# Performance work log

Measured on AMD Instinct MI355X. Metric: run time of the kernel, lower is better.

## Reference

```python
import jax, jax.numpy as jnp
import numpy as np

B, N_IN, D_IN = 64, 2304, 8
J, L = 32, 16  # num_capsules, capsule_dim
ROUTING_ITERS = 3
EPS = 1e-7


def setup_inputs() -> dict:
    key = jax.random.key(0)
    k1, k2 = jax.random.split(key)
    x = jax.random.normal(k1, (B, N_IN, D_IN), dtype=jnp.float32)
    W = jax.random.normal(k2, (N_IN, J, D_IN, L), dtype=jnp.float32) * 0.05
    return {"x": x, "W": W}


def squash(s):
    # s: [B, J, L]
    sq_norm = jnp.sum(jnp.square(s), axis=-1, keepdims=True)
    scale = sq_norm / (1.0 + sq_norm) / jnp.sqrt(sq_norm + EPS)
    return scale * s


def reference(x, W):
    # Faithful to the source: einsum 'bni,njkl->bnjl' sums i and k independently.
    predictions = jnp.einsum('bni,njkl->bnjl', x, W)  # [B, N, J, L]
    b = jnp.zeros((x.shape[0], N_IN, J), dtype=predictions.dtype)
    v = None
    for i in range(ROUTING_ITERS):
        c = jax.nn.softmax(b, axis=2)                       # [B, N, J]
        s = jnp.sum(predictions * c[..., None], axis=1)     # [B, J, L]
        v = squash(s)                                       # [B, J, L]
        if i < ROUTING_ITERS - 1:
            agreement = jnp.einsum('bnjl,bjl->bnj', predictions, v)
            b = b + agreement
    return v
```

## Files before the change

### kernel.cpp

```cpp
#include <hip/hip_runtime.h>

#define B_   64
#define N_   2304
#define J_   32
#define L_   16
#define EPS_ 1e-7f
#define BG   4
#define NSPL 16
#define NSL  144
#define NTHR 1024
#define NT   18
#define STR  20

__global__ __launch_bounds__(256) void prep_kernel(const float* __restrict__ x,
                                                   const float* __restrict__ W,
                                                   float* __restrict__ Ws,
                                                   float* __restrict__ xs_g) {
    const int o = blockIdx.x * 256 + threadIdx.x;
    const int NW4 = N_ * J_ * L_ / 4;
    if (o < NW4) {
        const int n = o >> 7, r = o & 127;
        const float4* base = (const float4*)W + (size_t)n * 1024 + (r >> 2) * 32 + (r & 3);
        float4 s = make_float4(0.f, 0.f, 0.f, 0.f);
#pragma unroll
        for (int k = 0; k < 8; ++k) {
            float4 t = base[k * 4];
            s.x += t.x; s.y += t.y; s.z += t.z; s.w += t.w;
        }
        ((float4*)Ws)[o] = s;
    } else {
        const int q = o - NW4;
        if (q < B_ * N_) {
            const float4* p4 = (const float4*)(x + (size_t)q * 8);
            float4 a = p4[0], c = p4[1];
            xs_g[q] = a.x + a.y + a.z + a.w + c.x + c.y + c.z + c.w;
        }
    }
}

template<int T>
__global__ __launch_bounds__(NTHR) void iter_kernel(const float* __restrict__ Ws,
                                                    const float* __restrict__ xs_g,
                                                    const float* __restrict__ pA,
                                                    const float* __restrict__ pB,
                                                    float* __restrict__ pout) {
    __shared__ float xs_lds[BG * NSL];
    __shared__ float u_lds[BG * 544];
    __shared__ float sred[512 * STR];

    const int tid = threadIdx.x;
    const int sp  = blockIdx.x & 15;
    const int bg  = blockIdx.x >> 4;
    const int bb  = bg * BG;
    const int nb  = sp * NSL;

    if (tid < BG * NSL) {
        const int b4f = tid / NSL, nlf = tid - b4f * NSL;
        xs_lds[tid] = xs_g[(size_t)(bb + b4f) * N_ + nb + nlf];
    }

    if constexpr (T > 0) {
        for (int q = tid; q < BG * 512; q += NTHR) {
            const int ob = q >> 9, jl = q & 511;
            const float* pp = pA + ((size_t)(bb + ob) * NSPL) * 512 + jl;
            float s = 0.f;
#pragma unroll
            for (int s2 = 0; s2 < NSPL; ++s2) s += pp[s2 * 512];
            float sq = s * s;
#pragma unroll
            for (int off = 1; off <= 8; off <<= 1) sq += __shfl_xor(sq, off);
            float u = s * (sq / (1.f + sq) / sqrtf(sq + EPS_));
            if constexpr (T == 2) {
                const float* pq = pB + ((size_t)(bb + ob) * NSPL) * 512 + jl;
                float s1 = 0.f;
#pragma unroll
                for (int s2 = 0; s2 < NSPL; ++s2) s1 += pq[s2 * 512];
                float sq1 = s1 * s1;
#pragma unroll
                for (int off = 1; off <= 8; off <<= 1) sq1 += __shfl_xor(sq1, off);
                u += s1 * (sq1 / (1.f + sq1) / sqrtf(sq1 + EPS_));
            }
            u_lds[ob * 544 + (jl >> 4) * 17 + (jl & 15)] = u;
        }
    }
    __syncthreads();

    const int nl8 = tid >> 7;
    const int b4  = (tid >> 5) & 3;
    const int j   = tid & 31;

    float u4[16];
    if constexpr (T > 0) {
#pragma unroll
        for (int l = 0; l < 16; ++l) u4[l] = u_lds[b4 * 544 + j * 17 + l];
    }

    float acc[16];
#pragma unroll
    for (int l = 0; l < 16; ++l) acc[l] = 0.f;

    const float* wbase = Ws + (size_t)nb * 512 + j * 16;
    const float* xbase = xs_lds + b4 * NSL;

    for (int tile = 0; tile < NT; ++tile) {
        const int nl = tile * 8 + nl8;
        const float4* wr = (const float4*)(wbase + (size_t)nl * 512);
        float4 w0 = wr[0], w1 = wr[1], w2 = wr[2], w3 = wr[3];
        const float xsv = xbase[nl];
        float wgt;
        if constexpr (T == 0) {
            wgt = xsv * (1.f / 32.f);
        } else {
            float lg = w0.x*u4[0]  + w0.y*u4[1]  + w0.z*u4[2]  + w0.w*u4[3]
                     + w1.x*u4[4]  + w1.y*u4[5]  + w1.z*u4[6]  + w1.w*u4[7]
                     + w2.x*u4[8]  + w2.y*u4[9]  + w2.z*u4[10] + w2.w*u4[11]
                     + w3.x*u4[12] + w3.y*u4[13] + w3.z*u4[14] + w3.w*u4[15];
            lg *= xsv;
            float e = __expf(lg);
            float ss = e;
#pragma unroll
            for (int off = 1; off <= 16; off <<= 1) ss += __shfl_xor(ss, off);
            wgt = (e / ss) * xsv;
        }
        acc[0]  += wgt*w0.x; acc[1]  += wgt*w0.y; acc[2]  += wgt*w0.z; acc[3]  += wgt*w0.w;
        acc[4]  += wgt*w1.x; acc[5]  += wgt*w1.y; acc[6]  += wgt*w1.z; acc[7]  += wgt*w1.w;
        acc[8]  += wgt*w2.x; acc[9]  += wgt*w2.y; acc[10] += wgt*w2.z; acc[11] += wgt*w2.w;
        acc[12] += wgt*w3.x; acc[13] += wgt*w3.y; acc[14] += wgt*w3.z; acc[15] += wgt*w3.w;
    }

    if (nl8 >= 4) {
        float* sr = sred + (size_t)(tid - 512) * STR;
        ((float4*)sr)[0] = make_float4(acc[0],  acc[1],  acc[2],  acc[3]);
        ((float4*)sr)[1] = make_float4(acc[4],  acc[5],  acc[6],  acc[7]);
        ((float4*)sr)[2] = make_float4(acc[8],  acc[9],  acc[10], acc[11]);
        ((float4*)sr)[3] = make_float4(acc[12], acc[13], acc[14], acc[15]);
    }
    __syncthreads();
    if (nl8 < 4) {
        float* sr = sred + (size_t)tid * STR;
#pragma unroll
        for (int d = 0; d < 4; ++d) {
            float4 t = ((float4*)sr)[d];
            t.x += acc[d*4+0]; t.y += acc[d*4+1]; t.z += acc[d*4+2]; t.w += acc[d*4+3];
            ((float4*)sr)[d] = t;
        }
    }
    __syncthreads();

    for (int q = tid; q < BG * 512; q += NTHR) {
        const int ob = q >> 9, jl = q & 511;
        const int oj = jl >> 4, ol = jl & 15;
        float s = 0.f;
#pragma unroll
        for (int nl = 0; nl < 4; ++nl)
            s += sred[(size_t)(nl * 128 + ob * 32 + oj) * STR + ol];
        pout[((size_t)(bb + ob) * NSPL + sp) * 512 + jl] = s;
    }
}

__global__ __launch_bounds__(512) void final_kernel(const float* __restrict__ p2,
                                                    float* __restrict__ out) {
    const int g = blockIdx.x * 512 + threadIdx.x;
    const int b = g >> 9, jl = g & 511;
    const float* pp = p2 + ((size_t)b * NSPL) * 512 + jl;
    float s = 0.f;
#pragma unroll
    for (int s2 = 0; s2 < NSPL; ++s2) s += pp[s2 * 512];
    float sq = s * s;
#pragma unroll
    for (int off = 1; off <= 8; off <<= 1) sq += __shfl_xor(sq, off);
    out[g] = s * (sq / (1.f + sq) / sqrtf(sq + EPS_));
}

extern "C" void kernel_launch(void* const* d_in, const int* in_sizes, int n_in,
                              void* d_out, int out_size, void* d_ws, size_t ws_size,
                              hipStream_t stream) {
    const float* x = (const float*)d_in[0];
    const float* W = (const float*)d_in[1];
    float* out = (float*)d_out;

    float* Ws  = (float*)d_ws;
    float* xsg = Ws  + (size_t)N_ * J_ * L_;
    float* p0  = xsg + (size_t)B_ * N_;
    float* p1  = p0  + (size_t)B_ * NSPL * 512;
    float* p2  = p1  + (size_t)B_ * NSPL * 512;

    prep_kernel<<<1728, 256, 0, stream>>>(x, W, Ws, xsg);
    iter_kernel<0><<<256, NTHR, 0, stream>>>(Ws, xsg, nullptr, nullptr, p0);
    iter_kernel<1><<<256, NTHR, 0, stream>>>(Ws, xsg, p0, nullptr, p1);
    iter_kernel<2><<<256, NTHR, 0, stream>>>(Ws, xsg, p0, p1, p2);
    final_kernel<<<64, 512, 0, stream>>>(p2, out);
}
```

Baseline: 78.09 us.

## Replace split partials with atomic accumulation and fuse final squash into last iteration

```diff
diff --git a/kernel.cpp b/kernel.cpp
--- a/kernel.cpp
+++ b/kernel.cpp
@@ -12,11 +12,14 @@
 #define NT   18
 #define STR  20
 
+
 __global__ __launch_bounds__(256) void prep_kernel(const float* __restrict__ x,
                                                    const float* __restrict__ W,
                                                    float* __restrict__ Ws,
-                                                   float* __restrict__ xs_g) {
+                                                   float* __restrict__ xs_g,
+                                                   float* __restrict__ zr) {
     const int o = blockIdx.x * 256 + threadIdx.x;
+    if (o < 2 * B_ * 512 + 1) zr[o] = 0.f;
     const int NW4 = N_ * J_ * L_ / 4;
     if (o < NW4) {
         const int n = o >> 7, r = o & 127;
@@ -41,12 +44,17 @@
 template<int T>
 __global__ __launch_bounds__(NTHR) void iter_kernel(const float* __restrict__ Ws,
                                                     const float* __restrict__ xs_g,
-                                                    const float* __restrict__ pA,
-                                                    const float* __restrict__ pB,
-                                                    float* __restrict__ pout) {
+                                                    const float* __restrict__ p0,
+                                                    float* __restrict__ s0g,
+                                                    float* __restrict__ s1g,
+                                                    float* __restrict__ s2g,
+                                                    int* __restrict__ ctr,
+                                                    float* __restrict__ pout,
+                                                    float* __restrict__ out) {
     __shared__ float xs_lds[BG * NSL];
     __shared__ float u_lds[BG * 544];
     __shared__ float sred[512 * STR];
+    __shared__ int lastflag;
 
     const int tid = threadIdx.x;
     const int sp  = blockIdx.x & 15;
@@ -59,27 +67,34 @@
         xs_lds[tid] = xs_g[(size_t)(bb + b4f) * N_ + nb + nlf];
     }
 
-    if constexpr (T > 0) {
+    if constexpr (T == 1) {
         for (int q = tid; q < BG * 512; q += NTHR) {
             const int ob = q >> 9, jl = q & 511;
-            const float* pp = pA + ((size_t)(bb + ob) * NSPL) * 512 + jl;
+            const float* pp = p0 + ((size_t)(bb + ob) * NSPL) * 512 + jl;
             float s = 0.f;
 #pragma unroll
-            for (int s2 = 0; s2 < NSPL; ++s2) s += pp[s2 * 512];
+            for (int s2i = 0; s2i < NSPL; ++s2i) s += pp[s2i * 512];
+            if (sp == 0) s0g[(bb + ob) * 512 + jl] = s;
+            float sq = s * s;
+#pragma unroll
+            for (int off = 1; off <= 8; off <<= 1) sq += __shfl_xor(sq, off);
+            u_lds[ob * 544 + (jl >> 4) * 17 + (jl & 15)] =
+                s * (sq / (1.f + sq) / sqrtf(sq + EPS_));
+        }
+    } else if constexpr (T == 2) {
+        for (int q = tid; q < BG * 512; q += NTHR) {
+            const int ob = q >> 9, jl = q & 511;
+            const int g = (bb + ob) * 512 + jl;
+            float s = s0g[g];
             float sq = s * s;
 #pragma unroll
             for (int off = 1; off <= 8; off <<= 1) sq += __shfl_xor(sq, off);
             float u = s * (sq / (1.f + sq) / sqrtf(sq + EPS_));
-            if constexpr (T == 2) {
-                const float* pq = pB + ((size_t)(bb + ob) * NSPL) * 512 + jl;
-                float s1 = 0.f;
-#pragma unroll
-                for (int s2 = 0; s2 < NSPL; ++s2) s1 += pq[s2 * 512];
-                float sq1 = s1 * s1;
-#pragma unroll
-                for (int off = 1; off <= 8; off <<= 1) sq1 += __shfl_xor(sq1, off);
-                u += s1 * (sq1 / (1.f + sq1) / sqrtf(sq1 + EPS_));
-            }
+            float s1 = s1g[g];
+            float sq1 = s1 * s1;
+#pragma unroll
+            for (int off = 1; off <= 8; off <<= 1) sq1 += __shfl_xor(sq1, off);
+            u += s1 * (sq1 / (1.f + sq1) / sqrtf(sq1 + EPS_));
             u_lds[ob * 544 + (jl >> 4) * 17 + (jl & 15)] = u;
         }
     }
@@ -154,22 +169,42 @@
 #pragma unroll
         for (int nl = 0; nl < 4; ++nl)
             s += sred[(size_t)(nl * 128 + ob * 32 + oj) * STR + ol];
-        pout[((size_t)(bb + ob) * NSPL + sp) * 512 + jl] = s;
-    }
-}
-
-__global__ __launch_bounds__(512) void final_kernel(const float* __restrict__ p2,
-                                                    float* __restrict__ out) {
-    const int g = blockIdx.x * 512 + threadIdx.x;
-    const int b = g >> 9, jl = g & 511;
-    const float* pp = p2 + ((size_t)b * NSPL) * 512 + jl;
-    float s = 0.f;
-#pragma unroll
-    for (int s2 = 0; s2 < NSPL; ++s2) s += pp[s2 * 512];
-    float sq = s * s;
-#pragma unroll
-    for (int off = 1; off <= 8; off <<= 1) sq += __shfl_xor(sq, off);
-    out[g] = s * (sq / (1.f + sq) / sqrtf(sq + EPS_));
+        if constexpr (T == 0)
+            pout[((size_t)(bb + ob) * NSPL + sp) * 512 + jl] = s;
+        else if constexpr (T == 1)
+            unsafeAtomicAdd(&s1g[(bb + ob) * 512 + jl], s);
+        else
+            unsafeAtomicAdd(&s2g[(bb + ob) * 512 + jl], s);
+    }
+
+    if constexpr (T == 2) {
+        __threadfence();
+        __syncthreads();
+        if (tid == 0) {
+            int old = __hip_atomic_fetch_add(ctr, 1, __ATOMIC_ACQ_REL,
+                                             __HIP_MEMORY_SCOPE_AGENT);
+            lastflag = (old == 255) ? 1 : 0;
+        }
+        __syncthreads();
+        if (lastflag) {
+            __threadfence();
+            for (int r = tid; r < B_ * J_; r += NTHR) {
+                const int b = r >> 5, jj = r & 31;
+                const float4* s4 = (const float4*)(s2g + b * 512 + jj * 16);
+                float4 a0 = s4[0], a1 = s4[1], a2 = s4[2], a3 = s4[3];
+                float sq = a0.x*a0.x + a0.y*a0.y + a0.z*a0.z + a0.w*a0.w
+                         + a1.x*a1.x + a1.y*a1.y + a1.z*a1.z + a1.w*a1.w
+                         + a2.x*a2.x + a2.y*a2.y + a2.z*a2.z + a2.w*a2.w
+                         + a3.x*a3.x + a3.y*a3.y + a3.z*a3.z + a3.w*a3.w;
+                const float sc = sq / (1.f + sq) / sqrtf(sq + EPS_);
+                float4* o4 = (float4*)(out + b * 512 + jj * 16);
+                o4[0] = make_float4(a0.x*sc, a0.y*sc, a0.z*sc, a0.w*sc);
+                o4[1] = make_float4(a1.x*sc, a1.y*sc, a1.z*sc, a1.w*sc);
+                o4[2] = make_float4(a2.x*sc, a2.y*sc, a2.z*sc, a2.w*sc);
+                o4[3] = make_float4(a3.x*sc, a3.y*sc, a3.z*sc, a3.w*sc);
+            }
+        }
+    }
 }
 
 extern "C" void kernel_launch(void* const* d_in, const int* in_sizes, int n_in,
@@ -182,12 +217,16 @@
     float* Ws  = (float*)d_ws;
     float* xsg = Ws  + (size_t)N_ * J_ * L_;
     float* p0  = xsg + (size_t)B_ * N_;
-    float* p1  = p0  + (size_t)B_ * NSPL * 512;
-    float* p2  = p1  + (size_t)B_ * NSPL * 512;
-
-    prep_kernel<<<1728, 256, 0, stream>>>(x, W, Ws, xsg);
-    iter_kernel<0><<<256, NTHR, 0, stream>>>(Ws, xsg, nullptr, nullptr, p0);
-    iter_kernel<1><<<256, NTHR, 0, stream>>>(Ws, xsg, p0, nullptr, p1);
-    iter_kernel<2><<<256, NTHR, 0, stream>>>(Ws, xsg, p0, p1, p2);
-    final_kernel<<<64, 512, 0, stream>>>(p2, out);
+    float* s0  = p0  + (size_t)B_ * NSPL * 512;
+    float* s1  = s0  + (size_t)B_ * 512;
+    float* s2  = s1  + (size_t)B_ * 512;
+    int*   ctr = (int*)(s2 + (size_t)B_ * 512);
+
+    prep_kernel<<<1728, 256, 0, stream>>>(x, W, Ws, xsg, s1);
+    iter_kernel<0><<<256, NTHR, 0, stream>>>(Ws, xsg, nullptr, nullptr, nullptr,
+                                             nullptr, nullptr, p0, nullptr);
+    iter_kernel<1><<<256, NTHR, 0, stream>>>(Ws, xsg, p0, s0, s1,
+                                             nullptr, nullptr, nullptr, nullptr);
+    iter_kernel<2><<<256, NTHR, 0, stream>>>(Ws, xsg, nullptr, s0, s1,
+                                             s2, ctr, nullptr, out);
 }
```

After: 146.1 us. 87.1% more time.
